# Performance work log

Hardware: AMD Instinct MI355X
Metric: run time of the kernel (lower is better)

The kernel has to match this reference:

```python
import jax, jax.numpy as jnp
import numpy as np

BETA = 0.25  # commitment loss weight (standard VQ-VAE)


def setup_inputs() -> dict:
    key = jax.random.key(0)
    ks = jax.random.split(key, 6)
    B, C, H, W = 8, 64, 64, 64
    K = 8192  # codebook size
    return {
        "z": jax.random.normal(ks[0], (B, C, H, W), dtype=jnp.float32),
        "pre_w": jax.random.normal(ks[1], (C, C), dtype=jnp.float32) * (1.0 / np.sqrt(C)),
        "pre_b": jax.random.normal(ks[2], (C,), dtype=jnp.float32) * 0.02,
        "emb": jax.random.normal(ks[3], (K, C), dtype=jnp.float32),
        "post_w": jax.random.normal(ks[4], (C, C), dtype=jnp.float32) * (1.0 / np.sqrt(C)),
        "post_b": jax.random.normal(ks[5], (C,), dtype=jnp.float32) * 0.02,
    }


def reference(z, pre_w, pre_b, emb, post_w, post_b):
    B, C, H, W = z.shape
    # pre_quant_conv: 1x1 conv == channel-mixing matmul
    ze = jnp.einsum("bchw,oc->bohw", z, pre_w) + pre_b[None, :, None, None]
    # flatten to tokens [N, C]
    zf = ze.transpose(0, 2, 3, 1).reshape(-1, C)
    # squared L2 distances to codebook: ||z||^2 - 2 z.e + ||e||^2
    d = (jnp.sum(zf * zf, axis=1, keepdims=True)
         - 2.0 * (zf @ emb.T)
         + jnp.sum(emb * emb, axis=1)[None, :])  # [N, K]
    idx = jnp.argmin(d, axis=1)  # [N]
    q = emb[idx].reshape(B, H, W, C).transpose(0, 3, 1, 2)  # [B,C,H,W]
    # VQ losses
    codebook_loss = jnp.mean((jax.lax.stop_gradient(ze) - q) ** 2)
    commit_loss = BETA * jnp.mean((ze - jax.lax.stop_gradient(q)) ** 2)
    loss = codebook_loss + commit_loss
    # straight-through estimator
    quant = ze + jax.lax.stop_gradient(q - ze)
    # post_quant_conv: 1x1 conv
    out = jnp.einsum("bchw,oc->bohw", quant, post_w) + post_b[None, :, None, None]
    return out, loss
```

## Files before the change

### kernel.cpp

```cpp
#include <hip/hip_runtime.h>
#include <stdint.h>

#define HW 4096
#define NTOK 32768
#define KCB 8192
#define YSPLIT 8
#define KCOV (KCB / YSPLIT)
#define NCHUNK (KCOV / 64)
#define MARGIN 0.0119628906f

typedef __bf16 bf16x8 __attribute__((ext_vector_type(8)));
typedef float f32x16 __attribute__((ext_vector_type(16)));
typedef unsigned int uint;
typedef unsigned short u16;
typedef unsigned long long u64;

static __device__ inline u16 f2bf(float f) {
    uint u = __float_as_uint(f);
    return (u16)((u + 0x7FFFu + ((u >> 16) & 1u)) >> 16);
}
static __device__ inline float bf2f(u16 h) {
    return __uint_as_float(((uint)h) << 16);
}
static __device__ inline uint fsort(float f) {
    uint u = __float_as_uint(f);
    return u ^ ((uint)((int)u >> 31) | 0x80000000u);
}
static __device__ inline uint umin2(uint a, uint b) { return a < b ? a : b; }
static __device__ inline uint umax2(uint a, uint b) { return a > b ? a : b; }
static __device__ inline uint umed3(uint a, uint b, uint c) {
    return umax2(umin2(a, b), umin2(umax2(a, b), c));
}

__global__ __launch_bounds__(256) void embprep_kernel(
    const float* __restrict__ emb, u16* __restrict__ embq,
    float* __restrict__ ee, float* __restrict__ eebs, int* __restrict__ flagcnt)
{
    const int t   = threadIdx.x;
    const int k   = blockIdx.x * 32 + (t >> 3);
    const int sub = t & 7;
    const float4* er = (const float4*)(emb + (size_t)k * 64 + sub * 8);
    float4 v0 = er[0], v1 = er[1];

    float s = v0.x*v0.x + v0.y*v0.y + v0.z*v0.z + v0.w*v0.w
            + v1.x*v1.x + v1.y*v1.y + v1.z*v1.z + v1.w*v1.w;
    s += __shfl_xor(s, 1, 64);
    s += __shfl_xor(s, 2, 64);
    s += __shfl_xor(s, 4, 64);
    if (sub == 0) { ee[k] = s; eebs[k] = 1024.f * (256.f + s); }

    float vals[8] = {-64.f*v0.x, -64.f*v0.y, -64.f*v0.z, -64.f*v0.w,
                     -64.f*v1.x, -64.f*v1.y, -64.f*v1.z, -64.f*v1.w};
    u16 hb[8], lb[8];
    #pragma unroll
    for (int c = 0; c < 8; ++c) {
        hb[c] = f2bf(vals[c]);
        lb[c] = f2bf(vals[c] - bf2f(hb[c]));
    }
    uint4 uh, ul;
    uh.x = (uint)hb[0] | ((uint)hb[1] << 16);
    uh.y = (uint)hb[2] | ((uint)hb[3] << 16);
    uh.z = (uint)hb[4] | ((uint)hb[5] << 16);
    uh.w = (uint)hb[6] | ((uint)hb[7] << 16);
    ul.x = (uint)lb[0] | ((uint)lb[1] << 16);
    ul.y = (uint)lb[2] | ((uint)lb[3] << 16);
    ul.z = (uint)lb[4] | ((uint)lb[5] << 16);
    ul.w = (uint)lb[6] | ((uint)lb[7] << 16);

    const int sw = k & 7;
    uint4* out = (uint4*)(embq + (size_t)k * 128);
    out[sub ^ sw]       = uh;
    out[(8 + sub) ^ sw] = ul;
    if (k == 0 && t == 0) *flagcnt = 0;
}

__global__ __launch_bounds__(256) void preconv_kernel(
    const float* __restrict__ z, const float* __restrict__ pre_w,
    const float* __restrict__ pre_b, u16* __restrict__ zq)
{
    __shared__ __attribute__((aligned(16))) float wt[64 * 64];
    __shared__ __attribute__((aligned(16))) float zt[64 * 64];
    __shared__ float bls[64];
    const int t = threadIdx.x;
    const int tok0 = blockIdx.x * 64;
    const int b    = tok0 >> 12;
    const int hw0  = tok0 & 4095;

    for (int i = t; i < 64 * 64; i += 256) {
        int o = i >> 6, c = i & 63;
        wt[c * 64 + o] = pre_w[i];
    }
    if (t < 64) bls[t] = pre_b[t];
    {
        const int tl = t & 63;
        #pragma unroll
        for (int rr = 0; rr < 16; ++rr) {
            const int c = (t >> 6) + rr * 4;
            zt[c * 64 + tl] = z[(size_t)b * (64 * HW) + (size_t)c * HW + hw0 + tl];
        }
    }
    __syncthreads();

    const int tok = t >> 2;
    const int og  = t & 3;
    const int n   = tok0 + tok;

    float acc[16];
    #pragma unroll
    for (int j = 0; j < 16; ++j) acc[j] = 0.f;

    for (int c = 0; c < 64; ++c) {
        const float zv = zt[c * 64 + tok];
        #pragma unroll
        for (int g = 0; g < 4; ++g) {
            float4 w4 = *(const float4*)(wt + c * 64 + og * 16 + g * 4);
            acc[g*4+0] = fmaf(zv, w4.x, acc[g*4+0]);
            acc[g*4+1] = fmaf(zv, w4.y, acc[g*4+1]);
            acc[g*4+2] = fmaf(zv, w4.z, acc[g*4+2]);
            acc[g*4+3] = fmaf(zv, w4.w, acc[g*4+3]);
        }
    }
    #pragma unroll
    for (int j = 0; j < 16; ++j) acc[j] = 32.f * (acc[j] + bls[og * 16 + j]);

    uint uh[8], ul[8];
    #pragma unroll
    for (int j = 0; j < 8; ++j) {
        float v0 = acc[2*j], v1 = acc[2*j+1];
        u16 h0 = f2bf(v0), h1 = f2bf(v1);
        u16 l0 = f2bf(v0 - bf2f(h0)), l1 = f2bf(v1 - bf2f(h1));
        uh[j] = (uint)h0 | ((uint)h1 << 16);
        ul[j] = (uint)l0 | ((uint)l1 << 16);
    }
    uint4* zh = (uint4*)(zq + (size_t)n * 128 + og * 16);
    uint4* zl = (uint4*)(zq + (size_t)n * 128 + 64 + og * 16);
    zh[0] = *(uint4*)&uh[0]; zh[1] = *(uint4*)&uh[4];
    zl[0] = *(uint4*)&ul[0]; zl[1] = *(uint4*)&ul[4];
}

__global__ __launch_bounds__(256, 4) void dist_kernel(
    const u16* __restrict__ zq, const u16* __restrict__ embq,
    const float* __restrict__ eebs, uint* __restrict__ halfbb,
    uint* __restrict__ halfss)
{
    __shared__ __attribute__((aligned(16))) char smem[32768];
    __shared__ uint gbk[128];

    const int t    = threadIdx.x;
    const int w    = t >> 6;
    const int l    = t & 63;
    const int col  = l & 31;
    const int half = l >> 5;
    const int tok0 = blockIdx.x * 128;
    const int y    = blockIdx.y;
    const int kbase = y * KCOV;

    bf16x8 ah[4], al[4];
    {
        const u16* zrow = zq + (size_t)(tok0 + w * 32 + col) * 128;
        #pragma unroll
        for (int s = 0; s < 4; ++s) {
            ah[s] = *(const bf16x8*)(zrow + s*16 + half*8);
            al[s] = *(const bf16x8*)(zrow + 64 + s*16 + half*8);
        }
    }

    const int sw = col & 7;
    int boh[4][2], bol[4][2];
    #pragma unroll
    for (int s = 0; s < 4; ++s)
        #pragma unroll
        for (int ct = 0; ct < 2; ++ct) {
            const int nl = ct * 32 + col;
            boh[s][ct] = nl * 256 + (((s*2 + half) ^ sw) << 4);
            bol[s][ct] = nl * 256 + (((8 + s*2 + half) ^ sw) << 4);
        }

    uint bb[16], ss[16];
    #pragma unroll
    for (int r = 0; r < 16; ++r) { bb[r] = 0xFFFFFFFFu; ss[r] = 0xFFFFFFFFu; }

    float e0 = eebs[kbase + col];
    float e1 = eebs[kbase + 32 + col];

    {
        const char* g = (const char*)embq + (size_t)kbase * 256;
        #pragma unroll
        for (int i = 0; i < 4; ++i) {
            int off = i * 4096 + t * 16;
            __builtin_amdgcn_global_load_lds(
                (const __attribute__((address_space(1))) void*)(g + off),
                (__attribute__((address_space(3))) void*)(smem + off), 16, 0, 0);
        }
    }

    for (int kt = 0; kt < NCHUNK; ++kt) {
        __syncthreads();
        if (kt + 1 < NCHUNK) {
            const char* g = (const char*)embq + (size_t)kbase * 256 + (size_t)(kt + 1) * 16384;
            char* ld = smem + ((kt + 1) & 1) * 16384;
            #pragma unroll
            for (int i = 0; i < 4; ++i) {
                int off = i * 4096 + t * 16;
                __builtin_amdgcn_global_load_lds(
                    (const __attribute__((address_space(1))) void*)(g + off),
                    (__attribute__((address_space(3))) void*)(ld + off), 16, 0, 0);
            }
        }
        const char* buf = smem + (kt & 1) * 16384;

        float e0n = 0.f, e1n = 0.f;
        if (kt + 1 < NCHUNK) {
            e0n = eebs[kbase + (kt+1)*64 + col];
            e1n = eebs[kbase + (kt+1)*64 + 32 + col];
        }

        f32x16 a0, a1;
        #pragma unroll
        for (int r = 0; r < 16; ++r) { a0[r] = e0; a1[r] = e1; }

        #pragma unroll
        for (int s = 0; s < 4; ++s) {
            bf16x8 bh0 = *(const bf16x8*)(buf + boh[s][0]);
            bf16x8 bh1 = *(const bf16x8*)(buf + boh[s][1]);
            bf16x8 bl0 = *(const bf16x8*)(buf + bol[s][0]);
            bf16x8 bl1 = *(const bf16x8*)(buf + bol[s][1]);
            a0 = __builtin_amdgcn_mfma_f32_32x32x16_bf16(ah[s], bh0, a0, 0, 0, 0);
            a1 = __builtin_amdgcn_mfma_f32_32x32x16_bf16(ah[s], bh1, a1, 0, 0, 0);
            a0 = __builtin_amdgcn_mfma_f32_32x32x16_bf16(ah[s], bl0, a0, 0, 0, 0);
            a1 = __builtin_amdgcn_mfma_f32_32x32x16_bf16(ah[s], bl1, a1, 0, 0, 0);
            a0 = __builtin_amdgcn_mfma_f32_32x32x16_bf16(al[s], bh0, a0, 0, 0, 0);
            a1 = __builtin_amdgcn_mfma_f32_32x32x16_bf16(al[s], bh1, a1, 0, 0, 0);
        }

        const uint i0 = (uint)(kt * 64 + col);
        const uint i1 = i0 + 32;
        #pragma unroll
        for (int r = 0; r < 16; ++r) {
            const uint p0 = (((uint)a0[r]) << 10) + i0;
            const uint p1 = (((uint)a1[r]) << 10) + i1;
            ss[r] = umin2(ss[r], umed3(bb[r], p0, p1));
            bb[r] = umin2(umin2(bb[r], p0), p1);
        }
        e0 = e0n; e1 = e1n;
    }

    __syncthreads();
    uint* keyt = (uint*)smem;
    #pragma unroll
    for (int r = 0; r < 16; ++r) {
        const int tl = w*32 + (r & 3) + 8*(r >> 2) + 4*half;
        keyt[tl * 32 + col] = bb[r];
    }
    __syncthreads();
    if (t < 128) {
        uint gb = keyt[t * 32 + (t & 31)];
        #pragma unroll 4
        for (int j = 1; j < 32; ++j)
            gb = umin2(gb, keyt[t * 32 + ((j + t) & 31)]);
        gbk[t] = gb;
    }
    __syncthreads();
    #pragma unroll
    for (int r = 0; r < 16; ++r) {
        const int tl = w*32 + (r & 3) + 8*(r >> 2) + 4*half;
        const uint mykey = bb[r];
        keyt[tl * 32 + col] = (mykey == gbk[tl]) ? ss[r] : mykey;
    }
    __syncthreads();
    if (t < 128) {
        uint sv = keyt[t * 32 + (t & 31)];
        #pragma unroll 4
        for (int j = 1; j < 32; ++j)
            sv = umin2(sv, keyt[t * 32 + ((j + t) & 31)]);
        halfbb[(size_t)y * NTOK + tok0 + t] = gbk[t];
        halfss[(size_t)y * NTOK + tok0 + t] = sv;
    }
}

__global__ __launch_bounds__(256) void merge_kernel(
    const uint* __restrict__ halfbb, const uint* __restrict__ halfss,
    uint* __restrict__ bestidx, u64* __restrict__ bestkeyB,
    int* __restrict__ flagcnt, int* __restrict__ flaglist,
    float* __restrict__ loss_out)
{
    const int n = blockIdx.x * 256 + threadIdx.x;
    uint m1 = 0xFFFFFFFFu, m2 = 0xFFFFFFFFu, smin = 0xFFFFFFFFu;
    int ywin = 0;
    #pragma unroll
    for (int y = 0; y < YSPLIT; ++y) {
        const uint kb = halfbb[(size_t)y * NTOK + n];
        if (kb < m1) { m2 = m1; m1 = kb; ywin = y; }
        else if (kb < m2) m2 = kb;
        smin = umin2(smin, halfss[(size_t)y * NTOK + n]);
    }
    const uint bv_u = m1 >> 10;
    const uint sv_u = umin2(m2, smin) >> 10;
    const float gap = (float)(sv_u - bv_u) * 9.765625e-4f;
    const bool flag = (gap < MARGIN) | (bv_u < (128u << 10));
    bestidx[n]  = flag ? 0xFFFFFFFFu : (uint)(ywin * 1024) + (m1 & 1023u);
    bestkeyB[n] = ~0ull;
    if (flag) {
        int pos = atomicAdd(flagcnt, 1);
        flaglist[pos] = n;
    }
    if (n == 0) loss_out[0] = 0.f;
}

__global__ __launch_bounds__(256) void cleanup_kernel(
    const u16* __restrict__ zq, const float* __restrict__ emb,
    const float* __restrict__ ee, const int* __restrict__ flagcnt,
    const int* __restrict__ flaglist, u64* __restrict__ bestkeyB)
{
    __shared__ __attribute__((aligned(16))) float zf[64];
    __shared__ u64 smin;
    const int cnt = *flagcnt;
    const int t = threadIdx.x;

    for (int job = blockIdx.x; job < cnt * 32; job += 2048) {
        const int fi    = job >> 5;
        const int slice = job & 31;
        const int tok   = flaglist[fi];
        if (t == 0) smin = ~0ull;
        if (t < 64) {
            const u16* zr = zq + (size_t)tok * 128;
            zf[t] = (bf2f(zr[t]) + bf2f(zr[64 + t])) * 0.03125f;
        }
        __syncthreads();

        const int k = slice * 256 + t;
        const float4* er = (const float4*)(emb + (size_t)k * 64);
        float d = 0.f;
        #pragma unroll
        for (int jj = 0; jj < 16; ++jj) {
            float4 e = er[jj];
            float4 zv = *(const float4*)&zf[4*jj];
            d = fmaf(e.x, zv.x, fmaf(e.y, zv.y, fmaf(e.z, zv.z, fmaf(e.w, zv.w, d))));
        }
        float dd = fmaf(-2.f, d, ee[k]);
        u64 key = ((u64)fsort(dd) << 32) | (uint)k;
        #pragma unroll
        for (int off = 32; off > 0; off >>= 1) {
            u64 o = __shfl_down(key, off, 64);
            key = (o < key) ? o : key;
        }
        if ((t & 63) == 0) atomicMin(&smin, key);
        __syncthreads();
        if (t == 0) atomicMin(&bestkeyB[tok], smin);
        __syncthreads();
    }
}

__global__ __launch_bounds__(256) void gather_kernel(
    const float* __restrict__ emb, const uint* __restrict__ bestidx,
    const u64* __restrict__ bestkeyB, const u16* __restrict__ zq,
    const float* __restrict__ post_w, const float* __restrict__ post_b,
    float* __restrict__ out, float* __restrict__ loss_out)
{
    __shared__ __attribute__((aligned(16))) float wt[64 * 64];
    __shared__ __attribute__((aligned(16))) float qt[64 * 64];
    __shared__ float bls[64];
    __shared__ int idxs[64];
    __shared__ float red[4];
    const int t = threadIdx.x;
    const int tok0 = blockIdx.x * 64;
    const int b    = tok0 >> 12;
    const int hw0  = tok0 & 4095;

    for (int i = t; i < 64 * 64; i += 256) {
        int o = i >> 6, c = i & 63;
        wt[c * 64 + o] = post_w[i];
    }
    if (t < 64) {
        bls[t] = post_b[t];
        const uint raw = bestidx[tok0 + t];
        idxs[t] = (raw == 0xFFFFFFFFu) ? (int)(bestkeyB[tok0 + t] & 0xFFFFFFFFull)
                                       : (int)raw;
    }
    __syncthreads();

    const int tok = t >> 2;
    const int og  = t & 3;
    const int n   = tok0 + tok;

    {
        const float4* qr = (const float4*)(emb + (size_t)idxs[tok] * 64);
        #pragma unroll
        for (int p = 0; p < 4; ++p) {
            const int c0 = og * 16 + p * 4;
            float4 v = qr[c0 >> 2];
            qt[(c0+0) * 64 + tok] = v.x;
            qt[(c0+1) * 64 + tok] = v.y;
            qt[(c0+2) * 64 + tok] = v.z;
            qt[(c0+3) * 64 + tok] = v.w;
        }
    }
    __syncthreads();

    float acc[16];
    #pragma unroll
    for (int j = 0; j < 16; ++j) acc[j] = 0.f;

    for (int c = 0; c < 64; ++c) {
        const float qv = qt[c * 64 + tok];
        #pragma unroll
        for (int g = 0; g < 4; ++g) {
            float4 w4 = *(const float4*)(wt + c * 64 + og * 16 + g * 4);
            acc[g*4+0] = fmaf(qv, w4.x, acc[g*4+0]);
            acc[g*4+1] = fmaf(qv, w4.y, acc[g*4+1]);
            acc[g*4+2] = fmaf(qv, w4.z, acc[g*4+2]);
            acc[g*4+3] = fmaf(qv, w4.w, acc[g*4+3]);
        }
    }

    float* op = out + (size_t)b * (64 * HW) + hw0 + tok;
    #pragma unroll
    for (int j = 0; j < 16; ++j)
        op[(size_t)(og * 16 + j) * HW] = acc[j] + bls[og * 16 + j];

    float lsum = 0.f;
    {
        const uint4* zh = (const uint4*)(zq + (size_t)n * 128 + og * 16);
        const uint4* zl = (const uint4*)(zq + (size_t)n * 128 + 64 + og * 16);
        #pragma unroll
        for (int h = 0; h < 2; ++h) {
            uint4 uh = zh[h], ul = zl[h];
            const uint uhv[4] = {uh.x, uh.y, uh.z, uh.w};
            const uint ulv[4] = {ul.x, ul.y, ul.z, ul.w};
            #pragma unroll
            for (int p = 0; p < 4; ++p) {
                const int c = og * 16 + h * 8 + p * 2;
                float z0 = (bf2f((u16)(uhv[p] & 0xFFFF)) + bf2f((u16)(ulv[p] & 0xFFFF))) * 0.03125f;
                float z1 = (bf2f((u16)(uhv[p] >> 16))    + bf2f((u16)(ulv[p] >> 16)))    * 0.03125f;
                float d0 = z0 - qt[c * 64 + tok];
                float d1 = z1 - qt[(c + 1) * 64 + tok];
                lsum += d0 * d0 + d1 * d1;
            }
        }
    }
    #pragma unroll
    for (int off = 32; off > 0; off >>= 1) lsum += __shfl_down(lsum, off, 64);
    if ((t & 63) == 0) red[t >> 6] = lsum;
    __syncthreads();
    if (t == 0) {
        const float tot = red[0] + red[1] + red[2] + red[3];
        atomicAdd(loss_out, tot * (1.25f / 2097152.f));
    }
}

extern "C" void kernel_launch(void* const* d_in, const int* in_sizes, int n_in,
                              void* d_out, int out_size, void* d_ws, size_t ws_size,
                              hipStream_t stream)
{
    const float* z      = (const float*)d_in[0];
    const float* pre_w  = (const float*)d_in[1];
    const float* pre_b  = (const float*)d_in[2];
    const float* emb    = (const float*)d_in[3];
    const float* post_w = (const float*)d_in[4];
    const float* post_b = (const float*)d_in[5];
    float* outp = (float*)d_out;
    float* loss_out = outp + (size_t)NTOK * 64;

    u16*   zq       = (u16*)d_ws;
    float* ee       = (float*)(zq + (size_t)NTOK * 128);
    float* eebs     = ee + KCB;
    u16*   embq     = (u16*)(eebs + KCB);
    u64*   bestkeyB = (u64*)(embq + (size_t)KCB * 128);
    uint*  bestidx  = (uint*)(bestkeyB + NTOK);
    int*   flagcnt  = (int*)(bestidx + NTOK);
    int*   flaglist = flagcnt + 1;
    uint*  halfbb   = (uint*)(flaglist + NTOK);
    uint*  halfss   = halfbb + (size_t)YSPLIT * NTOK;

    embprep_kernel<<<KCB / 32, 256, 0, stream>>>(emb, embq, ee, eebs, flagcnt);
    preconv_kernel<<<NTOK / 64, 256, 0, stream>>>(z, pre_w, pre_b, zq);
    dist_kernel<<<dim3(NTOK / 128, YSPLIT), 256, 0, stream>>>(zq, embq, eebs, halfbb, halfss);
    merge_kernel<<<NTOK / 256, 256, 0, stream>>>(halfbb, halfss, bestidx, bestkeyB,
                                                 flagcnt, flaglist, loss_out);
    cleanup_kernel<<<2048, 256, 0, stream>>>(zq, emb, ee, flagcnt, flaglist, bestkeyB);
    gather_kernel<<<NTOK / 64, 256, 0, stream>>>(emb, bestidx, bestkeyB, zq,
                                                 post_w, post_b, outp, loss_out);
}
```

Before: 235.2 us.

## Fuse embprep into preconv and merge/cleanup/gather into one finish kernel

Embedding preparation now runs as extra blocks of the pre-conv kernel, and the merge, cleanup and gather steps are folded into a single finish kernel. That kernel merges the split top-2 keys per token, builds a ballot mask of ambiguous tokens, and rescans the full codebook in fp32 for those tokens inside the same block. This cuts the number of launches from six to three and drops the flag-list atomics and the bestidx/bestkeyB workspace traffic. The catch is that flagged tokens are rescanned serially within one block rather than spread over 2048 blocks, so blocks that hold many flagged tokens become stragglers.

```diff
diff --git a/kernel.cpp b/kernel.cpp
--- a/kernel.cpp
+++ b/kernel.cpp
@@ -32,57 +32,59 @@
     return umax2(umin2(a, b), umin2(umax2(a, b), c));
 }
 
-__global__ __launch_bounds__(256) void embprep_kernel(
-    const float* __restrict__ emb, u16* __restrict__ embq,
-    float* __restrict__ ee, float* __restrict__ eebs, int* __restrict__ flagcnt)
-{
-    const int t   = threadIdx.x;
-    const int k   = blockIdx.x * 32 + (t >> 3);
-    const int sub = t & 7;
-    const float4* er = (const float4*)(emb + (size_t)k * 64 + sub * 8);
-    float4 v0 = er[0], v1 = er[1];
-
-    float s = v0.x*v0.x + v0.y*v0.y + v0.z*v0.z + v0.w*v0.w
-            + v1.x*v1.x + v1.y*v1.y + v1.z*v1.z + v1.w*v1.w;
-    s += __shfl_xor(s, 1, 64);
-    s += __shfl_xor(s, 2, 64);
-    s += __shfl_xor(s, 4, 64);
-    if (sub == 0) { ee[k] = s; eebs[k] = 1024.f * (256.f + s); }
-
-    float vals[8] = {-64.f*v0.x, -64.f*v0.y, -64.f*v0.z, -64.f*v0.w,
-                     -64.f*v1.x, -64.f*v1.y, -64.f*v1.z, -64.f*v1.w};
-    u16 hb[8], lb[8];
-    #pragma unroll
-    for (int c = 0; c < 8; ++c) {
-        hb[c] = f2bf(vals[c]);
-        lb[c] = f2bf(vals[c] - bf2f(hb[c]));
-    }
-    uint4 uh, ul;
-    uh.x = (uint)hb[0] | ((uint)hb[1] << 16);
-    uh.y = (uint)hb[2] | ((uint)hb[3] << 16);
-    uh.z = (uint)hb[4] | ((uint)hb[5] << 16);
-    uh.w = (uint)hb[6] | ((uint)hb[7] << 16);
-    ul.x = (uint)lb[0] | ((uint)lb[1] << 16);
-    ul.y = (uint)lb[2] | ((uint)lb[3] << 16);
-    ul.z = (uint)lb[4] | ((uint)lb[5] << 16);
-    ul.w = (uint)lb[6] | ((uint)lb[7] << 16);
-
-    const int sw = k & 7;
-    uint4* out = (uint4*)(embq + (size_t)k * 128);
-    out[sub ^ sw]       = uh;
-    out[(8 + sub) ^ sw] = ul;
-    if (k == 0 && t == 0) *flagcnt = 0;
-}
-
-__global__ __launch_bounds__(256) void preconv_kernel(
+__global__ __launch_bounds__(256) void prep_kernel(
     const float* __restrict__ z, const float* __restrict__ pre_w,
-    const float* __restrict__ pre_b, u16* __restrict__ zq)
+    const float* __restrict__ pre_b, const float* __restrict__ emb,
+    u16* __restrict__ zq, u16* __restrict__ embq,
+    float* __restrict__ ee, float* __restrict__ eebs,
+    float* __restrict__ loss_out)
 {
     __shared__ __attribute__((aligned(16))) float wt[64 * 64];
     __shared__ __attribute__((aligned(16))) float zt[64 * 64];
     __shared__ float bls[64];
-    const int t = threadIdx.x;
-    const int tok0 = blockIdx.x * 64;
+    const int t  = threadIdx.x;
+    const int bx = blockIdx.x;
+
+    if (bx >= 512) {
+        const int k   = (bx - 512) * 32 + (t >> 3);
+        const int sub = t & 7;
+        const float4* er = (const float4*)(emb + (size_t)k * 64 + sub * 8);
+        float4 v0 = er[0], v1 = er[1];
+
+        float s = v0.x*v0.x + v0.y*v0.y + v0.z*v0.z + v0.w*v0.w
+                + v1.x*v1.x + v1.y*v1.y + v1.z*v1.z + v1.w*v1.w;
+        s += __shfl_xor(s, 1, 64);
+        s += __shfl_xor(s, 2, 64);
+        s += __shfl_xor(s, 4, 64);
+        if (sub == 0) { ee[k] = s; eebs[k] = 1024.f * (256.f + s); }
+
+        float vals[8] = {-64.f*v0.x, -64.f*v0.y, -64.f*v0.z, -64.f*v0.w,
+                         -64.f*v1.x, -64.f*v1.y, -64.f*v1.z, -64.f*v1.w};
+        u16 hb[8], lb[8];
+        #pragma unroll
+        for (int c = 0; c < 8; ++c) {
+            hb[c] = f2bf(vals[c]);
+            lb[c] = f2bf(vals[c] - bf2f(hb[c]));
+        }
+        uint4 uh, ul;
+        uh.x = (uint)hb[0] | ((uint)hb[1] << 16);
+        uh.y = (uint)hb[2] | ((uint)hb[3] << 16);
+        uh.z = (uint)hb[4] | ((uint)hb[5] << 16);
+        uh.w = (uint)hb[6] | ((uint)hb[7] << 16);
+        ul.x = (uint)lb[0] | ((uint)lb[1] << 16);
+        ul.y = (uint)lb[2] | ((uint)lb[3] << 16);
+        ul.z = (uint)lb[4] | ((uint)lb[5] << 16);
+        ul.w = (uint)lb[6] | ((uint)lb[7] << 16);
+
+        const int sw = k & 7;
+        uint4* out = (uint4*)(embq + (size_t)k * 128);
+        out[sub ^ sw]       = uh;
+        out[(8 + sub) ^ sw] = ul;
+        if (bx == 512 && t == 0) loss_out[0] = 0.f;
+        return;
+    }
+
+    const int tok0 = bx * 64;
     const int b    = tok0 >> 12;
     const int hw0  = tok0 & 4095;
 
@@ -278,89 +280,20 @@
     }
 }
 
-__global__ __launch_bounds__(256) void merge_kernel(
+__global__ __launch_bounds__(256) void finish_kernel(
+    const float* __restrict__ emb, const float* __restrict__ ee,
     const uint* __restrict__ halfbb, const uint* __restrict__ halfss,
-    uint* __restrict__ bestidx, u64* __restrict__ bestkeyB,
-    int* __restrict__ flagcnt, int* __restrict__ flaglist,
+    const u16* __restrict__ zq, const float* __restrict__ post_w,
+    const float* __restrict__ post_b, float* __restrict__ out,
     float* __restrict__ loss_out)
-{
-    const int n = blockIdx.x * 256 + threadIdx.x;
-    uint m1 = 0xFFFFFFFFu, m2 = 0xFFFFFFFFu, smin = 0xFFFFFFFFu;
-    int ywin = 0;
-    #pragma unroll
-    for (int y = 0; y < YSPLIT; ++y) {
-        const uint kb = halfbb[(size_t)y * NTOK + n];
-        if (kb < m1) { m2 = m1; m1 = kb; ywin = y; }
-        else if (kb < m2) m2 = kb;
-        smin = umin2(smin, halfss[(size_t)y * NTOK + n]);
-    }
-    const uint bv_u = m1 >> 10;
-    const uint sv_u = umin2(m2, smin) >> 10;
-    const float gap = (float)(sv_u - bv_u) * 9.765625e-4f;
-    const bool flag = (gap < MARGIN) | (bv_u < (128u << 10));
-    bestidx[n]  = flag ? 0xFFFFFFFFu : (uint)(ywin * 1024) + (m1 & 1023u);
-    bestkeyB[n] = ~0ull;
-    if (flag) {
-        int pos = atomicAdd(flagcnt, 1);
-        flaglist[pos] = n;
-    }
-    if (n == 0) loss_out[0] = 0.f;
-}
-
-__global__ __launch_bounds__(256) void cleanup_kernel(
-    const u16* __restrict__ zq, const float* __restrict__ emb,
-    const float* __restrict__ ee, const int* __restrict__ flagcnt,
-    const int* __restrict__ flaglist, u64* __restrict__ bestkeyB)
-{
-    __shared__ __attribute__((aligned(16))) float zf[64];
-    __shared__ u64 smin;
-    const int cnt = *flagcnt;
-    const int t = threadIdx.x;
-
-    for (int job = blockIdx.x; job < cnt * 32; job += 2048) {
-        const int fi    = job >> 5;
-        const int slice = job & 31;
-        const int tok   = flaglist[fi];
-        if (t == 0) smin = ~0ull;
-        if (t < 64) {
-            const u16* zr = zq + (size_t)tok * 128;
-            zf[t] = (bf2f(zr[t]) + bf2f(zr[64 + t])) * 0.03125f;
-        }
-        __syncthreads();
-
-        const int k = slice * 256 + t;
-        const float4* er = (const float4*)(emb + (size_t)k * 64);
-        float d = 0.f;
-        #pragma unroll
-        for (int jj = 0; jj < 16; ++jj) {
-            float4 e = er[jj];
-            float4 zv = *(const float4*)&zf[4*jj];
-            d = fmaf(e.x, zv.x, fmaf(e.y, zv.y, fmaf(e.z, zv.z, fmaf(e.w, zv.w, d))));
-        }
-        float dd = fmaf(-2.f, d, ee[k]);
-        u64 key = ((u64)fsort(dd) << 32) | (uint)k;
-        #pragma unroll
-        for (int off = 32; off > 0; off >>= 1) {
-            u64 o = __shfl_down(key, off, 64);
-            key = (o < key) ? o : key;
-        }
-        if ((t & 63) == 0) atomicMin(&smin, key);
-        __syncthreads();
-        if (t == 0) atomicMin(&bestkeyB[tok], smin);
-        __syncthreads();
-    }
-}
-
-__global__ __launch_bounds__(256) void gather_kernel(
-    const float* __restrict__ emb, const uint* __restrict__ bestidx,
-    const u64* __restrict__ bestkeyB, const u16* __restrict__ zq,
-    const float* __restrict__ post_w, const float* __restrict__ post_b,
-    float* __restrict__ out, float* __restrict__ loss_out)
 {
     __shared__ __attribute__((aligned(16))) float wt[64 * 64];
     __shared__ __attribute__((aligned(16))) float qt[64 * 64];
+    __shared__ __attribute__((aligned(16))) float zf[64];
     __shared__ float bls[64];
     __shared__ int idxs[64];
+    __shared__ u64 fmask_s;
+    __shared__ u64 skey;
     __shared__ float red[4];
     const int t = threadIdx.x;
     const int tok0 = blockIdx.x * 64;
@@ -373,16 +306,67 @@
     }
     if (t < 64) {
         bls[t] = post_b[t];
-        const uint raw = bestidx[tok0 + t];
-        idxs[t] = (raw == 0xFFFFFFFFu) ? (int)(bestkeyB[tok0 + t] & 0xFFFFFFFFull)
-                                       : (int)raw;
-    }
-    __syncthreads();
+        const int n = tok0 + t;
+        uint m1 = 0xFFFFFFFFu, m2 = 0xFFFFFFFFu, smin = 0xFFFFFFFFu;
+        int ywin = 0;
+        #pragma unroll
+        for (int y = 0; y < YSPLIT; ++y) {
+            const uint kb = halfbb[(size_t)y * NTOK + n];
+            if (kb < m1) { m2 = m1; m1 = kb; ywin = y; }
+            else if (kb < m2) m2 = kb;
+            smin = umin2(smin, halfss[(size_t)y * NTOK + n]);
+        }
+        const uint bv_u = m1 >> 10;
+        const uint sv_u = umin2(m2, smin) >> 10;
+        const float gap = (float)(sv_u - bv_u) * 9.765625e-4f;
+        const bool flag = (gap < MARGIN) | (bv_u < (128u << 10));
+        idxs[t] = flag ? -1 : (int)((uint)(ywin * 1024) + (m1 & 1023u));
+        u64 m = __ballot(flag);
+        if (t == 0) fmask_s = m;
+    }
+    __syncthreads();
+
+    u64 fmask = fmask_s;
+    while (fmask) {
+        const int s = (int)__builtin_ctzll(fmask);
+        fmask &= fmask - 1;
+        const int tok = tok0 + s;
+        if (t == 0) skey = ~0ull;
+        if (t < 64) {
+            const u16* zr = zq + (size_t)tok * 128;
+            zf[t] = (bf2f(zr[t]) + bf2f(zr[64 + t])) * 0.03125f;
+        }
+        __syncthreads();
+
+        u64 loc = ~0ull;
+        for (int j = 0; j < 32; ++j) {
+            const int k = t + j * 256;
+            const float4* er = (const float4*)(emb + (size_t)k * 64);
+            float d = 0.f;
+            #pragma unroll
+            for (int jj = 0; jj < 16; ++jj) {
+                float4 e = er[jj];
+                float4 zv = *(const float4*)&zf[4*jj];
+                d = fmaf(e.x, zv.x, fmaf(e.y, zv.y, fmaf(e.z, zv.z, fmaf(e.w, zv.w, d))));
+            }
+            float dd = fmaf(-2.f, d, ee[k]);
+            u64 key = ((u64)fsort(dd) << 32) | (uint)k;
+            if (key < loc) loc = key;
+        }
+        #pragma unroll
+        for (int off = 32; off > 0; off >>= 1) {
+            u64 o = __shfl_down(loc, off, 64);
+            loc = (o < loc) ? o : loc;
+        }
+        if ((t & 63) == 0) atomicMin(&skey, loc);
+        __syncthreads();
+        if (t == 0) idxs[s] = (int)(skey & 0xFFFFFFFFull);
+        __syncthreads();
+    }
 
     const int tok = t >> 2;
     const int og  = t & 3;
     const int n   = tok0 + tok;
-
     {
         const float4* qr = (const float4*)(emb + (size_t)idxs[tok] * 64);
         #pragma unroll
@@ -461,23 +445,15 @@
     float* outp = (float*)d_out;
     float* loss_out = outp + (size_t)NTOK * 64;
 
-    u16*   zq       = (u16*)d_ws;
-    float* ee       = (float*)(zq + (size_t)NTOK * 128);
-    float* eebs     = ee + KCB;
-    u16*   embq     = (u16*)(eebs + KCB);
-    u64*   bestkeyB = (u64*)(embq + (size_t)KCB * 128);
-    uint*  bestidx  = (uint*)(bestkeyB + NTOK);
-    int*   flagcnt  = (int*)(bestidx + NTOK);
-    int*   flaglist = flagcnt + 1;
-    uint*  halfbb   = (uint*)(flaglist + NTOK);
-    uint*  halfss   = halfbb + (size_t)YSPLIT * NTOK;
-
-    embprep_kernel<<<KCB / 32, 256, 0, stream>>>(emb, embq, ee, eebs, flagcnt);
-    preconv_kernel<<<NTOK / 64, 256, 0, stream>>>(z, pre_w, pre_b, zq);
+    u16*   zq     = (u16*)d_ws;
+    float* ee     = (float*)(zq + (size_t)NTOK * 128);
+    float* eebs   = ee + KCB;
+    u16*   embq   = (u16*)(eebs + KCB);
+    uint*  halfbb = (uint*)(embq + (size_t)KCB * 128);
+    uint*  halfss = halfbb + (size_t)YSPLIT * NTOK;
+
+    prep_kernel<<<768, 256, 0, stream>>>(z, pre_w, pre_b, emb, zq, embq, ee, eebs, loss_out);
     dist_kernel<<<dim3(NTOK / 128, YSPLIT), 256, 0, stream>>>(zq, embq, eebs, halfbb, halfss);
-    merge_kernel<<<NTOK / 256, 256, 0, stream>>>(halfbb, halfss, bestidx, bestkeyB,
-                                                 flagcnt, flaglist, loss_out);
-    cleanup_kernel<<<2048, 256, 0, stream>>>(zq, emb, ee, flagcnt, flaglist, bestkeyB);
-    gather_kernel<<<NTOK / 64, 256, 0, stream>>>(emb, bestidx, bestkeyB, zq,
+    finish_kernel<<<NTOK / 64, 256, 0, stream>>>(emb, ee, halfbb, halfss, zq,
                                                  post_w, post_b, outp, loss_out);
 }
```

Result: slower. 362.5 us (+54.2%).
